# Performance work log

Hardware: AMD Instinct MI355X
Metric: run time of the kernel (lower is better)

## Reference

```python
import jax, jax.numpy as jnp
import numpy as np

N_NODES = 100000
N_EDGES = 1600000
IN_DIM, HIDDEN_DIM, OUT_DIM = 64, 128, 40


def setup_inputs() -> dict:
    key = jax.random.key(0)
    k1, k2, k3, k4 = jax.random.split(key, 4)
    x = jax.random.normal(k1, (N_NODES, IN_DIM), dtype=jnp.float32)
    edge_index = jax.random.randint(k2, (2, N_EDGES), 0, N_NODES, dtype=jnp.int64)
    W1 = jax.random.normal(k3, (IN_DIM, HIDDEN_DIM), dtype=jnp.float32) * 0.05
    b1 = jnp.zeros((HIDDEN_DIM,), dtype=jnp.float32)
    W2 = jax.random.normal(k4, (HIDDEN_DIM, OUT_DIM), dtype=jnp.float32) * 0.05
    b2 = jnp.zeros((OUT_DIM,), dtype=jnp.float32)
    return {"x": x, "edge_index": edge_index, "W1": W1, "b1": b1, "W2": W2, "b2": b2}


def reference(x, edge_index, W1, b1, W2, b2):
    # PyG GINConv with default eps=0: out = nn(x_i + sum_{j in N(i)} x_j)
    src = edge_index[0]
    dst = edge_index[1]
    n = x.shape[0]

    def gin_layer(h, W, b):
        aggr = jax.ops.segment_sum(h[src], dst, num_segments=n)  # scatter-add of neighbor feats
        return (h + aggr) @ W + b

    h = jax.nn.relu(gin_layer(x, W1, b1))
    # dropout is identity in eval mode (training=False)
    h = gin_layer(h, W2, b2)
    return jax.nn.log_softmax(h, axis=1)
```

## Files before the change

### kernel.cpp

```cpp
#include <hip/hip_runtime.h>
#include <math.h>


#define IN_DIM 64
#define HID_DIM 128
#define OUT_DIM 40

#define BSH 8
#define MAXNB 512
#define EPB 4096
#define CAP 5120
#define H1S 136

typedef unsigned short ushort;
typedef unsigned char uchar;
typedef unsigned int uint;
typedef float floatx2 __attribute__((ext_vector_type(2)));
typedef short short8_t __attribute__((ext_vector_type(8)));
typedef float float4_t __attribute__((ext_vector_type(4)));

__device__ __forceinline__ ushort f2bf(float f) {
  unsigned u = __float_as_uint(f);
  u += 0x7fffu + ((u >> 16) & 1u);
  return (ushort)(u >> 16);
}


__global__ __launch_bounds__(256) void prep(
    const float4* __restrict__ x4, uint2* __restrict__ x8, int n8,
    const float* __restrict__ W1, const float* __restrict__ W2,
    ushort* __restrict__ W1T, ushort* __restrict__ W2T, int* __restrict__ gcur) {
  int id = blockIdx.x * 256 + threadIdx.x;
  if (id < n8) {
    float4 a = x4[2 * id], b = x4[2 * id + 1];
    int p0 = __builtin_amdgcn_cvt_pk_fp8_f32(a.x, a.y, 0, false);
    p0 = __builtin_amdgcn_cvt_pk_fp8_f32(a.z, a.w, p0, true);
    int p1 = __builtin_amdgcn_cvt_pk_fp8_f32(b.x, b.y, 0, false);
    p1 = __builtin_amdgcn_cvt_pk_fp8_f32(b.z, b.w, p1, true);
    x8[id] = (uint2){(uint)p0, (uint)p1};
  }
  if (id < HID_DIM * IN_DIM) {
    int c = id / IN_DIM, k = id - c * IN_DIM;
    W1T[id] = f2bf(W1[k * HID_DIM + c]);
  }
  if (id < 48 * HID_DIM) {
    int c = id / HID_DIM, k = id - c * HID_DIM;
    W2T[id] = (c < OUT_DIM) ? f2bf(W2[k * OUT_DIM + c]) : 0;
  }
  if (id < MAXNB) gcur[id] = 0;
}


__global__ __launch_bounds__(256) void bucket_scatter(
    const int* __restrict__ src, const int* __restrict__ dst,
    int* __restrict__ gcur, int* __restrict__ epk_s, int n_edges, int nb) {
  __shared__ int hist[MAXNB];
  __shared__ int lexcl[MAXNB];
  __shared__ int lofs[MAXNB];
  __shared__ int gbase[MAXNB];
  __shared__ int spk[EPB];
  __shared__ ushort sbid[EPB];
  int tid = threadIdx.x;
  for (int i = tid; i < nb; i += 256) { hist[i] = 0; lofs[i] = 0; }
  __syncthreads();
  int e0 = blockIdx.x * EPB;
  int cnt = min(EPB, n_edges - e0);
  for (int i = tid; i < cnt; i += 256) atomicAdd(&hist[dst[e0 + i] >> BSH], 1);
  __syncthreads();
  if (tid < 64) {
    int carry = 0;
    for (int c = 0; c < nb; c += 64) {
      int v = (c + tid < nb) ? hist[c + tid] : 0;
      int incl = v;
#pragma unroll
      for (int d = 1; d < 64; d <<= 1) {
        int t = __shfl_up(incl, d, 64);
        if (tid >= d) incl += t;
      }
      if (c + tid < nb) lexcl[c + tid] = carry + incl - v;
      carry += __shfl(incl, 63, 64);
    }
  }
  __syncthreads();
  for (int i = tid; i < nb; i += 256)
    if (hist[i]) gbase[i] = atomicAdd(&gcur[i], hist[i]);
  __syncthreads();
  for (int i = tid; i < cnt; i += 256) {
    int d = dst[e0 + i], s = src[e0 + i];
    int b = d >> BSH;
    int p = lexcl[b] + atomicAdd(&lofs[b], 1);
    spk[p] = ((d & 255) << 17) | s;
    sbid[p] = (ushort)b;
  }
  __syncthreads();
  for (int i = tid; i < cnt; i += 256) {
    int b = sbid[i];
    epk_s[b * CAP + gbase[b] + (i - lexcl[b])] = spk[i];
  }
}


__global__ __launch_bounds__(256) void bucket_csr(
    const int* __restrict__ epk_s, const int* __restrict__ gcnt,
    int2* __restrict__ off2, int* __restrict__ esrc_s, int n_nodes) {
  __shared__ int hist[256];
  __shared__ int cur[256];
  int b = blockIdx.x;
  int base = b * CAP;
  int cnt = gcnt[b];
  int nb0 = b << BSH;
  int nn = min(256, n_nodes - nb0);
  int tid = threadIdx.x;
  hist[tid] = 0;
  __syncthreads();
  for (int i = tid; i < cnt; i += 256) atomicAdd(&hist[epk_s[base + i] >> 17], 1);
  __syncthreads();
  if (tid < 64) {
    int carry = 0;
#pragma unroll
    for (int c = 0; c < 256; c += 64) {
      int v = hist[c + tid];
      int incl = v;
#pragma unroll
      for (int d = 1; d < 64; d <<= 1) {
        int t = __shfl_up(incl, d, 64);
        if (tid >= d) incl += t;
      }
      cur[c + tid] = carry + incl - v;
      carry += __shfl(incl, 63, 64);
    }
  }
  __syncthreads();
  if (tid < nn) {
    int st = cur[tid];
    off2[nb0 + tid] = make_int2(base + st, base + st + hist[tid]);
  }
  __syncthreads();
  for (int i = tid; i < cnt; i += 256) {
    int p = epk_s[base + i];
    int pos = atomicAdd(&cur[p >> 17], 1);
    esrc_s[base + pos] = p & 0x1FFFF;
  }
}


__global__ __launch_bounds__(256) void agg1(
    const float4* __restrict__ x4, const uint* __restrict__ x8,
    const int2* __restrict__ off2, const int* __restrict__ esrc,
    ushort* __restrict__ aggrh, int n_nodes) {
  int tid = threadIdx.x;
  int lane = tid & 63;
  int nsel = (lane >> 5) & 1, es = (lane >> 4) & 1, q = lane & 15;
  int node = blockIdx.x * 8 + (tid >> 6) * 2 + nsel;
  bool nok = node < n_nodes;
  int2 oe = nok ? off2[node] : make_int2(0, 0);
  float4 xo = nok ? x4[(uint)(node * 16 + q)] : (float4){0.f, 0.f, 0.f, 0.f};
  floatx2 A0 = {0.f, 0.f}, A1 = {0.f, 0.f};
  floatx2 C0 = {0.f, 0.f}, C1 = {0.f, 0.f};
  int e = oe.x, end = oe.y;
  for (; e + 4 <= end; e += 4) {
    uint u0 = x8[(uint)(esrc[e + es] * 16 + q)];
    uint u1 = x8[(uint)(esrc[e + es + 2] * 16 + q)];
    A0 += __builtin_amdgcn_cvt_pk_f32_fp8((int)u0, false);
    A1 += __builtin_amdgcn_cvt_pk_f32_fp8((int)u0, true);
    C0 += __builtin_amdgcn_cvt_pk_f32_fp8((int)u1, false);
    C1 += __builtin_amdgcn_cvt_pk_f32_fp8((int)u1, true);
  }
  for (; e < end; e += 2) {
    int idx = e + es;
    if (idx < end) {
      uint u = x8[(uint)(esrc[idx] * 16 + q)];
      A0 += __builtin_amdgcn_cvt_pk_f32_fp8((int)u, false);
      A1 += __builtin_amdgcn_cvt_pk_f32_fp8((int)u, true);
    }
  }
  A0 += C0; A1 += C1;
  {
    floatx2 t0, t1;
    t0[0] = __shfl_xor(A0[0], 16, 64); t0[1] = __shfl_xor(A0[1], 16, 64);
    t1[0] = __shfl_xor(A1[0], 16, 64); t1[1] = __shfl_xor(A1[1], 16, 64);
    A0 += t0; A1 += t1;
  }
  A0 += (floatx2){xo.x, xo.y};
  A1 += (floatx2){xo.z, xo.w};
  if (nok && es == 0) {
    uint2 o;
    o.x = (uint)f2bf(A0[0]) | ((uint)f2bf(A0[1]) << 16);
    o.y = (uint)f2bf(A1[0]) | ((uint)f2bf(A1[1]) << 16);
    ((uint2*)aggrh)[(uint)(node * 16 + q)] = o;
  }
}


__global__ __launch_bounds__(256) void gemm12_mfma(
    const ushort* __restrict__ aggrh, const ushort* __restrict__ W1T,
    const float* __restrict__ b1, const ushort* __restrict__ W2T,
    uchar* __restrict__ th8, int n_nodes) {
  __shared__ ushort h1s[64 * H1S];
  int w = threadIdx.x >> 6, lane = threadIdx.x & 63;
  int n0 = blockIdx.x * 64 + w * 16;
  int row = lane & 15, kg = lane >> 4;
  int n = n0 + row;
  {
    short8_t a0 = {}, a1 = {};
    if (n < n_nodes) {
      a0 = *(const short8_t*)&aggrh[(size_t)n * IN_DIM + kg * 8];
      a1 = *(const short8_t*)&aggrh[(size_t)n * IN_DIM + 32 + kg * 8];
    }
    float4_t acc[8];
#pragma unroll
    for (int ct = 0; ct < 8; ++ct) acc[ct] = (float4_t){0.f, 0.f, 0.f, 0.f};
#pragma unroll
    for (int ct = 0; ct < 8; ++ct) {
      int c = ct * 16 + row;
      short8_t b0 = *(const short8_t*)&W1T[(size_t)c * IN_DIM + kg * 8];
      short8_t b1f = *(const short8_t*)&W1T[(size_t)c * IN_DIM + 32 + kg * 8];
      acc[ct] = __builtin_amdgcn_mfma_f32_16x16x32_bf16(a0, b0, acc[ct], 0, 0, 0);
      acc[ct] = __builtin_amdgcn_mfma_f32_16x16x32_bf16(a1, b1f, acc[ct], 0, 0, 0);
    }
#pragma unroll
    for (int ct = 0; ct < 8; ++ct) {
      int j = ct * 16 + row;
      float bias = b1[j];
#pragma unroll
      for (int i = 0; i < 4; ++i) {
        int nl = w * 16 + kg * 4 + i;
        h1s[nl * H1S + j] = f2bf(fmaxf(acc[ct][i] + bias, 0.f));
      }
    }
  }
  __syncthreads();
  {
    short8_t a[4];
#pragma unroll
    for (int ks = 0; ks < 4; ++ks)
      a[ks] = *(const short8_t*)&h1s[(w * 16 + row) * H1S + ks * 32 + kg * 8];
    float4_t acc[3];
#pragma unroll
    for (int ct = 0; ct < 3; ++ct) acc[ct] = (float4_t){0.f, 0.f, 0.f, 0.f};
#pragma unroll
    for (int ct = 0; ct < 3; ++ct) {
      int c = ct * 16 + row;
#pragma unroll
      for (int ks = 0; ks < 4; ++ks) {
        short8_t b = *(const short8_t*)&W2T[(size_t)c * HID_DIM + ks * 32 + kg * 8];
        acc[ct] = __builtin_amdgcn_mfma_f32_16x16x32_bf16(a[ks], b, acc[ct], 0, 0, 0);
      }
    }
#pragma unroll
    for (int ct = 0; ct < 3; ++ct) {
      int j = ct * 16 + row;
      if (j < OUT_DIM) {
#pragma unroll
        for (int i = 0; i < 4; ++i) {
          int nn = n0 + kg * 4 + i;
          if (nn < n_nodes) {
            int pk = __builtin_amdgcn_cvt_pk_fp8_f32(acc[ct][i], acc[ct][i], 0, false);
            th8[(size_t)nn * 40 + j] = (uchar)(pk & 0xff);
          }
        }
      }
    }
  }
}


__global__ __launch_bounds__(256) void final_fused(
    const uchar* __restrict__ th8, const int2* __restrict__ off2,
    const int* __restrict__ esrc, const float* __restrict__ b2,
    float* __restrict__ out, int n_nodes) {
  int tid = threadIdx.x;
  int lane = tid & 63;
  int nsel = (lane >> 5) & 1, es = (lane >> 4) & 1, q = lane & 15;
  int node = blockIdx.x * 8 + (tid >> 6) * 2 + nsel;
  bool nok = node < n_nodes;
  bool valid = nok && (q < 10);
  const uint* tr = (const uint*)th8;
  int2 oe = nok ? off2[node] : make_int2(0, 0);
  uint uown = 0;
  float4 bb = {0.f, 0.f, 0.f, 0.f};
  if (valid) {
    uown = tr[(uint)(node * 10 + q)];
    bb = ((const float4*)b2)[q];
  }
  floatx2 A01 = {0.f, 0.f}, A23 = {0.f, 0.f};
  floatx2 C01 = {0.f, 0.f}, C23 = {0.f, 0.f};
  int e = oe.x, end = oe.y;
  for (; e + 4 <= end; e += 4) {
    uint u0 = 0, u1 = 0;
    if (valid) {
      u0 = tr[(uint)(esrc[e + es] * 10 + q)];
      u1 = tr[(uint)(esrc[e + es + 2] * 10 + q)];
    }
    A01 += __builtin_amdgcn_cvt_pk_f32_fp8((int)u0, false);
    A23 += __builtin_amdgcn_cvt_pk_f32_fp8((int)u0, true);
    C01 += __builtin_amdgcn_cvt_pk_f32_fp8((int)u1, false);
    C23 += __builtin_amdgcn_cvt_pk_f32_fp8((int)u1, true);
  }
  for (; e < end; e += 2) {
    int idx = e + es;
    if (idx < end && valid) {
      uint u = tr[(uint)(esrc[idx] * 10 + q)];
      A01 += __builtin_amdgcn_cvt_pk_f32_fp8((int)u, false);
      A23 += __builtin_amdgcn_cvt_pk_f32_fp8((int)u, true);
    }
  }
  A01 += C01; A23 += C23;
  {
    floatx2 t0, t1;
    t0[0] = __shfl_xor(A01[0], 16, 64); t0[1] = __shfl_xor(A01[1], 16, 64);
    t1[0] = __shfl_xor(A23[0], 16, 64); t1[1] = __shfl_xor(A23[1], 16, 64);
    A01 += t0; A23 += t1;
  }
  A01 += __builtin_amdgcn_cvt_pk_f32_fp8((int)uown, false);
  A23 += __builtin_amdgcn_cvt_pk_f32_fp8((int)uown, true);
  A01 += (floatx2){bb.x, bb.y};
  A23 += (floatx2){bb.z, bb.w};
  float m = valid ? fmaxf(fmaxf(A01[0], A01[1]), fmaxf(A23[0], A23[1])) : -INFINITY;
#pragma unroll
  for (int d = 1; d <= 8; d <<= 1) m = fmaxf(m, __shfl_xor(m, d, 64));
  float ssum = 0.f;
  if (valid)
    ssum = (__expf(A01[0] - m) + __expf(A01[1] - m)) +
           (__expf(A23[0] - m) + __expf(A23[1] - m));
#pragma unroll
  for (int d = 1; d <= 8; d <<= 1) ssum += __shfl_xor(ssum, d, 64);
  if (valid && es == 0) {
    float ls = m + __logf(ssum);
    float4 o = {A01[0] - ls, A01[1] - ls, A23[0] - ls, A23[1] - ls};
    ((float4*)out)[(uint)(node * 10 + q)] = o;
  }
}


static inline char* align256(char* p) {
  return (char*)(((uintptr_t)p + 255) & ~(uintptr_t)255);
}

extern "C" void kernel_launch(void* const* d_in, const int* in_sizes, int n_in,
                              void* d_out, int out_size, void* d_ws, size_t ws_size,
                              hipStream_t stream) {
  const float* x  = (const float*)d_in[0];
  const int*   ei = (const int*)d_in[1];
  const float* W1 = (const float*)d_in[2];
  const float* b1 = (const float*)d_in[3];
  const float* W2 = (const float*)d_in[4];
  const float* b2 = (const float*)d_in[5];
  float* out = (float*)d_out;

  int n_nodes = in_sizes[0] / IN_DIM;
  int n_edges = in_sizes[1] / 2;
  const int* src = ei;
  const int* dst = ei + n_edges;
  int nb = (n_nodes + 255) >> BSH;

  char* p = (char*)d_ws;
  int* gcur   = (int*)p;            p += MAXNB * 4;
  int2* off2  = (int2*)p;           p += (size_t)n_nodes * 8;
  p = align256(p);
  int* epk_s  = (int*)p;            p += (size_t)nb * CAP * 4;
  int* esrc_s = (int*)p;            p += (size_t)nb * CAP * 4;
  p = align256(p);
  uchar* x8    = (uchar*)p;         p += (size_t)n_nodes * IN_DIM;
  p = align256(p);
  ushort* aggrh = (ushort*)p;       p += (size_t)n_nodes * IN_DIM * 2;
  p = align256(p);
  uchar* th8    = (uchar*)p;        p += (size_t)n_nodes * 40 + 256;
  p = align256(p);
  ushort* W1T   = (ushort*)p;       p += HID_DIM * IN_DIM * 2;
  ushort* W2T   = (ushort*)p;       p += 48 * HID_DIM * 2;

  int n8 = n_nodes * IN_DIM / 8;
  prep<<<(n8 + 255) / 256, 256, 0, stream>>>(
      (const float4*)x, (uint2*)x8, n8, W1, W2, W1T, W2T, gcur);

  int egrid = (n_edges + EPB - 1) / EPB;
  bucket_scatter<<<egrid, 256, 0, stream>>>(src, dst, gcur, epk_s, n_edges, nb);
  bucket_csr<<<nb, 256, 0, stream>>>(epk_s, gcur, off2, esrc_s, n_nodes);

  agg1<<<(n_nodes + 7) / 8, 256, 0, stream>>>(
      (const float4*)x, (const uint*)x8, off2, esrc_s, aggrh, n_nodes);
  int ggrid = (n_nodes + 63) / 64;
  gemm12_mfma<<<ggrid, 256, 0, stream>>>(aggrh, W1T, b1, W2T, th8, n_nodes);
  final_fused<<<(n_nodes + 7) / 8, 256, 0, stream>>>(th8, off2, esrc_s, b2, out, n_nodes);
}
```

Baseline: 148.6 us.

## Fuse layer-1 aggregation into the MFMA GEMM kernel via shared memory

```diff
diff --git a/kernel.cpp b/kernel.cpp
--- a/kernel.cpp
+++ b/kernel.cpp
@@ -10,6 +10,7 @@
 #define MAXNB 512
 #define EPB 4096
 #define CAP 5120
+#define AGS 72
 #define H1S 136
 
 typedef unsigned short ushort;
@@ -144,69 +145,72 @@
 }
 
 
-__global__ __launch_bounds__(256) void agg1(
+__global__ __launch_bounds__(256) void agg_gemm12(
     const float4* __restrict__ x4, const uint* __restrict__ x8,
     const int2* __restrict__ off2, const int* __restrict__ esrc,
-    ushort* __restrict__ aggrh, int n_nodes) {
+    const ushort* __restrict__ W1T, const float* __restrict__ b1,
+    const ushort* __restrict__ W2T, uchar* __restrict__ th8, int n_nodes) {
+  __shared__ ushort aggs[64 * AGS];
+  __shared__ ushort h1s[64 * H1S];
   int tid = threadIdx.x;
-  int lane = tid & 63;
-  int nsel = (lane >> 5) & 1, es = (lane >> 4) & 1, q = lane & 15;
-  int node = blockIdx.x * 8 + (tid >> 6) * 2 + nsel;
-  bool nok = node < n_nodes;
-  int2 oe = nok ? off2[node] : make_int2(0, 0);
-  float4 xo = nok ? x4[(uint)(node * 16 + q)] : (float4){0.f, 0.f, 0.f, 0.f};
-  floatx2 A0 = {0.f, 0.f}, A1 = {0.f, 0.f};
-  floatx2 C0 = {0.f, 0.f}, C1 = {0.f, 0.f};
-  int e = oe.x, end = oe.y;
-  for (; e + 4 <= end; e += 4) {
-    uint u0 = x8[(uint)(esrc[e + es] * 16 + q)];
-    uint u1 = x8[(uint)(esrc[e + es + 2] * 16 + q)];
-    A0 += __builtin_amdgcn_cvt_pk_f32_fp8((int)u0, false);
-    A1 += __builtin_amdgcn_cvt_pk_f32_fp8((int)u0, true);
-    C0 += __builtin_amdgcn_cvt_pk_f32_fp8((int)u1, false);
-    C1 += __builtin_amdgcn_cvt_pk_f32_fp8((int)u1, true);
-  }
-  for (; e < end; e += 2) {
-    int idx = e + es;
-    if (idx < end) {
-      uint u = x8[(uint)(esrc[idx] * 16 + q)];
-      A0 += __builtin_amdgcn_cvt_pk_f32_fp8((int)u, false);
-      A1 += __builtin_amdgcn_cvt_pk_f32_fp8((int)u, true);
-    }
-  }
-  A0 += C0; A1 += C1;
+  int w = tid >> 6, lane = tid & 63;
+  int n0 = blockIdx.x * 64;
   {
-    floatx2 t0, t1;
-    t0[0] = __shfl_xor(A0[0], 16, 64); t0[1] = __shfl_xor(A0[1], 16, 64);
-    t1[0] = __shfl_xor(A1[0], 16, 64); t1[1] = __shfl_xor(A1[1], 16, 64);
-    A0 += t0; A1 += t1;
-  }
-  A0 += (floatx2){xo.x, xo.y};
-  A1 += (floatx2){xo.z, xo.w};
-  if (nok && es == 0) {
-    uint2 o;
-    o.x = (uint)f2bf(A0[0]) | ((uint)f2bf(A0[1]) << 16);
-    o.y = (uint)f2bf(A1[0]) | ((uint)f2bf(A1[1]) << 16);
-    ((uint2*)aggrh)[(uint)(node * 16 + q)] = o;
-  }
-}
-
-
-__global__ __launch_bounds__(256) void gemm12_mfma(
-    const ushort* __restrict__ aggrh, const ushort* __restrict__ W1T,
-    const float* __restrict__ b1, const ushort* __restrict__ W2T,
-    uchar* __restrict__ th8, int n_nodes) {
-  __shared__ ushort h1s[64 * H1S];
-  int w = threadIdx.x >> 6, lane = threadIdx.x & 63;
-  int n0 = blockIdx.x * 64 + w * 16;
+    int nsel = (lane >> 5) & 1, es = (lane >> 4) & 1, q = lane & 15;
+#pragma unroll
+    for (int r = 0; r < 8; ++r) {
+      int nl = w * 16 + r * 2 + nsel;
+      int node = n0 + nl;
+      bool nok = node < n_nodes;
+      int2 oe = nok ? off2[node] : make_int2(0, 0);
+      float4 xo = nok ? x4[(uint)(node * 16 + q)] : (float4){0.f, 0.f, 0.f, 0.f};
+      floatx2 A0 = {0.f, 0.f}, A1 = {0.f, 0.f};
+      floatx2 C0 = {0.f, 0.f}, C1 = {0.f, 0.f};
+      int e = oe.x, end = oe.y;
+      for (; e + 8 <= end; e += 8) {
+        uint u0 = x8[(uint)(esrc[e + es] * 16 + q)];
+        uint u1 = x8[(uint)(esrc[e + es + 2] * 16 + q)];
+        uint u2 = x8[(uint)(esrc[e + es + 4] * 16 + q)];
+        uint u3 = x8[(uint)(esrc[e + es + 6] * 16 + q)];
+        A0 += __builtin_amdgcn_cvt_pk_f32_fp8((int)u0, false);
+        A1 += __builtin_amdgcn_cvt_pk_f32_fp8((int)u0, true);
+        C0 += __builtin_amdgcn_cvt_pk_f32_fp8((int)u1, false);
+        C1 += __builtin_amdgcn_cvt_pk_f32_fp8((int)u1, true);
+        A0 += __builtin_amdgcn_cvt_pk_f32_fp8((int)u2, false);
+        A1 += __builtin_amdgcn_cvt_pk_f32_fp8((int)u2, true);
+        C0 += __builtin_amdgcn_cvt_pk_f32_fp8((int)u3, false);
+        C1 += __builtin_amdgcn_cvt_pk_f32_fp8((int)u3, true);
+      }
+      for (; e < end; e += 2) {
+        int idx = e + es;
+        if (idx < end) {
+          uint u = x8[(uint)(esrc[idx] * 16 + q)];
+          A0 += __builtin_amdgcn_cvt_pk_f32_fp8((int)u, false);
+          A1 += __builtin_amdgcn_cvt_pk_f32_fp8((int)u, true);
+        }
+      }
+      A0 += C0; A1 += C1;
+      {
+        floatx2 t0, t1;
+        t0[0] = __shfl_xor(A0[0], 16, 64); t0[1] = __shfl_xor(A0[1], 16, 64);
+        t1[0] = __shfl_xor(A1[0], 16, 64); t1[1] = __shfl_xor(A1[1], 16, 64);
+        A0 += t0; A1 += t1;
+      }
+      A0 += (floatx2){xo.x, xo.y};
+      A1 += (floatx2){xo.z, xo.w};
+      if (es == 0) {
+        uint2 o;
+        o.x = (uint)f2bf(A0[0]) | ((uint)f2bf(A0[1]) << 16);
+        o.y = (uint)f2bf(A1[0]) | ((uint)f2bf(A1[1]) << 16);
+        *(uint2*)&aggs[nl * AGS + q * 4] = o;
+      }
+    }
+  }
+  __syncthreads();
   int row = lane & 15, kg = lane >> 4;
-  int n = n0 + row;
   {
-    short8_t a0 = {}, a1 = {};
-    if (n < n_nodes) {
-      a0 = *(const short8_t*)&aggrh[(size_t)n * IN_DIM + kg * 8];
-      a1 = *(const short8_t*)&aggrh[(size_t)n * IN_DIM + 32 + kg * 8];
-    }
+    short8_t a0 = *(const short8_t*)&aggs[(w * 16 + row) * AGS + kg * 8];
+    short8_t a1 = *(const short8_t*)&aggs[(w * 16 + row) * AGS + 32 + kg * 8];
     float4_t acc[8];
 #pragma unroll
     for (int ct = 0; ct < 8; ++ct) acc[ct] = (float4_t){0.f, 0.f, 0.f, 0.f};
@@ -253,7 +257,7 @@
       if (j < OUT_DIM) {
 #pragma unroll
         for (int i = 0; i < 4; ++i) {
-          int nn = n0 + kg * 4 + i;
+          int nn = n0 + w * 16 + kg * 4 + i;
           if (nn < n_nodes) {
             int pk = __builtin_amdgcn_cvt_pk_fp8_f32(acc[ct][i], acc[ct][i], 0, false);
             th8[(size_t)nn * 40 + j] = (uchar)(pk & 0xff);
@@ -286,16 +290,22 @@
   floatx2 A01 = {0.f, 0.f}, A23 = {0.f, 0.f};
   floatx2 C01 = {0.f, 0.f}, C23 = {0.f, 0.f};
   int e = oe.x, end = oe.y;
-  for (; e + 4 <= end; e += 4) {
-    uint u0 = 0, u1 = 0;
+  for (; e + 8 <= end; e += 8) {
+    uint u0 = 0, u1 = 0, u2 = 0, u3 = 0;
     if (valid) {
       u0 = tr[(uint)(esrc[e + es] * 10 + q)];
       u1 = tr[(uint)(esrc[e + es + 2] * 10 + q)];
+      u2 = tr[(uint)(esrc[e + es + 4] * 10 + q)];
+      u3 = tr[(uint)(esrc[e + es + 6] * 10 + q)];
     }
     A01 += __builtin_amdgcn_cvt_pk_f32_fp8((int)u0, false);
     A23 += __builtin_amdgcn_cvt_pk_f32_fp8((int)u0, true);
     C01 += __builtin_amdgcn_cvt_pk_f32_fp8((int)u1, false);
     C23 += __builtin_amdgcn_cvt_pk_f32_fp8((int)u1, true);
+    A01 += __builtin_amdgcn_cvt_pk_f32_fp8((int)u2, false);
+    A23 += __builtin_amdgcn_cvt_pk_f32_fp8((int)u2, true);
+    C01 += __builtin_amdgcn_cvt_pk_f32_fp8((int)u3, false);
+    C23 += __builtin_amdgcn_cvt_pk_f32_fp8((int)u3, true);
   }
   for (; e < end; e += 2) {
     int idx = e + es;
@@ -363,12 +373,10 @@
   p = align256(p);
   uchar* x8    = (uchar*)p;         p += (size_t)n_nodes * IN_DIM;
   p = align256(p);
-  ushort* aggrh = (ushort*)p;       p += (size_t)n_nodes * IN_DIM * 2;
+  uchar* th8   = (uchar*)p;         p += (size_t)n_nodes * 40 + 256;
   p = align256(p);
-  uchar* th8    = (uchar*)p;        p += (size_t)n_nodes * 40 + 256;
-  p = align256(p);
-  ushort* W1T   = (ushort*)p;       p += HID_DIM * IN_DIM * 2;
-  ushort* W2T   = (ushort*)p;       p += 48 * HID_DIM * 2;
+  ushort* W1T  = (ushort*)p;        p += HID_DIM * IN_DIM * 2;
+  ushort* W2T  = (ushort*)p;        p += 48 * HID_DIM * 2;
 
   int n8 = n_nodes * IN_DIM / 8;
   prep<<<(n8 + 255) / 256, 256, 0, stream>>>(
@@ -378,9 +386,8 @@
   bucket_scatter<<<egrid, 256, 0, stream>>>(src, dst, gcur, epk_s, n_edges, nb);
   bucket_csr<<<nb, 256, 0, stream>>>(epk_s, gcur, off2, esrc_s, n_nodes);
 
-  agg1<<<(n_nodes + 7) / 8, 256, 0, stream>>>(
-      (const float4*)x, (const uint*)x8, off2, esrc_s, aggrh, n_nodes);
   int ggrid = (n_nodes + 63) / 64;
-  gemm12_mfma<<<ggrid, 256, 0, stream>>>(aggrh, W1T, b1, W2T, th8, n_nodes);
+  agg_gemm12<<<ggrid, 256, 0, stream>>>(
+      (const float4*)x, (const uint*)x8, off2, esrc_s, W1T, b1, W2T, th8, n_nodes);
   final_fused<<<(n_nodes + 7) / 8, 256, 0, stream>>>(th8, off2, esrc_s, b2, out, n_nodes);
 }
```

After: 158.2 us. 1.06x slower.
